# Kernel tuning notes

Hardware: AMD Instinct MI355X
Metric: run time of the kernel (lower is better)

## Reference

```python
import jax, jax.numpy as jnp
import numpy as np

D_MODEL = 2048
N_HEAD = 16
HEAD_DIM = D_MODEL // N_HEAD
SCALE = 1.0 / (HEAD_DIM ** 0.5)


def setup_inputs() -> dict:
    key = jax.random.key(0)
    kx, kq, kk, kv, ko = jax.random.split(key, 5)
    std = 1.0 / np.sqrt(D_MODEL)
    return {
        "x": jax.random.normal(kx, (2, 2048, D_MODEL), dtype=jnp.float32),
        "w_q": jax.random.normal(kq, (D_MODEL, D_MODEL), dtype=jnp.float32) * std,
        "w_k": jax.random.normal(kk, (D_MODEL, D_MODEL), dtype=jnp.float32) * std,
        "w_v": jax.random.normal(kv, (D_MODEL, D_MODEL), dtype=jnp.float32) * std,
        "w_o": jax.random.normal(ko, (D_MODEL, D_MODEL), dtype=jnp.float32) * std,
    }


def reference(x, w_q, w_k, w_v, w_o):
    b, s, d = x.shape
    # nn.Linear(d,d,bias=False): y = x @ W^T, weights stored [out, in]
    def proj(w):
        y = jnp.einsum("bsd,ed->bse", x, w)
        return y.reshape(b, s, N_HEAD, HEAD_DIM).transpose(0, 2, 1, 3)  # [b,h,s,hd]
    q, k, v = proj(w_q), proj(w_k), proj(w_v)
    scores = jnp.einsum("bhqd,bhkd->bhqk", q, k) * SCALE  # [b,h,s,s]
    probs = jax.nn.softmax(scores, axis=-1)
    attn = jnp.einsum("bhqk,bhkd->bhqd", probs, v)
    attn = attn.transpose(0, 2, 1, 3).reshape(b, s, d)
    return jnp.einsum("bsd,ed->bse", attn, w_o)
```

## Files before the change

### kernel.cpp

```cpp
#include <hip/hip_runtime.h>

#define D_MODEL 2048
#define SEQ 2048
#define BATCH 2
#define NH 16
#define HD 128
#define MTOT 4096
#define NQKV 6144
#define QSTRIDE 4096

static constexpr float SCALE_LOG2E = 0.08838834764831845f * 1.4426950408889634f;

typedef __bf16 bf16x8 __attribute__((ext_vector_type(8)));
typedef _Float16 f16x4 __attribute__((ext_vector_type(4)));
typedef float f32x4 __attribute__((ext_vector_type(4)));

__device__ inline unsigned short f2bf(float f) {
  unsigned int u = __builtin_bit_cast(unsigned int, f);
  u += 0x7fffu + ((u >> 16) & 1u);
  return (unsigned short)(u >> 16);
}

__device__ inline float fast_exp2(float x) {
#if __has_builtin(__builtin_amdgcn_exp2f)
  return __builtin_amdgcn_exp2f(x);
#else
  return exp2f(x);
#endif
}

__device__ inline void gload_lds16(const void* g, void* s) {
  __builtin_amdgcn_global_load_lds(
      (__attribute__((address_space(1))) void*)g,
      (__attribute__((address_space(3))) void*)s, 16, 0, 0);
}

__global__ __launch_bounds__(256) void cvt_all(
    const float* __restrict__ x, const float* __restrict__ wq,
    const float* __restrict__ wk, const float* __restrict__ wv,
    const float* __restrict__ wo, unsigned short* __restrict__ xb,
    unsigned short* __restrict__ wqkv, unsigned short* __restrict__ wob) {
  const int y = blockIdx.y;
  const float* src;
  unsigned short* dst;
  int n4;
  if (y == 0) { src = x; dst = xb; n4 = MTOT * D_MODEL / 4; }
  else if (y == 4) { src = wo; dst = wob; n4 = D_MODEL * D_MODEL / 4; }
  else {
    src = (y == 1) ? wq : (y == 2) ? wk : wv;
    dst = wqkv + (size_t)(y - 1) * D_MODEL * D_MODEL;
    n4 = D_MODEL * D_MODEL / 4;
  }
  int i = blockIdx.x * 256 + threadIdx.x;
  if (i < n4) {
    float4 v = ((const float4*)src)[i];
    ushort4 o;
    o.x = f2bf(v.x); o.y = f2bf(v.y); o.z = f2bf(v.z); o.w = f2bf(v.w);
    ((ushort4*)dst)[i] = o;
  }
}

__global__ __launch_bounds__(256, 2) void gemm_qkv(
    const unsigned short* __restrict__ A, const unsigned short* __restrict__ B,
    unsigned short* __restrict__ QK, unsigned short* __restrict__ Vt) {
  __shared__ __align__(16) union {
    struct { unsigned short As[128 * 32]; unsigned short Bs[128 * 32]; } s;
    unsigned short T[128 * 136];
  } u;
  unsigned short* As = u.s.As;
  unsigned short* Bs = u.s.Bs;
  const int K = D_MODEL;
  const int tid = threadIdx.x;
  const int lane = tid & 63;
  const int wave = tid >> 6;
  const int quad = lane >> 4;
  const int l15 = lane & 15;
  const int m0 = blockIdx.y * 128;
  const int n0 = blockIdx.x * 128;
  const int wm = (wave >> 1) * 64;
  const int wn = (wave & 1) * 64;

  const int c0 = wave * 2, c1 = wave * 2 + 1;
  const int srow = lane >> 2;
  const int sr0 = c0 * 16 + srow;
  const int sr1 = c1 * 16 + srow;
  const int sk = (((lane & 3) ^ (srow & 3))) * 8;
  const unsigned short* Ag0 = A + (size_t)(m0 + sr0) * K + sk;
  const unsigned short* Ag1 = A + (size_t)(m0 + sr1) * K + sk;
  const unsigned short* Bg0 = B + (size_t)(n0 + sr0) * K + sk;
  const unsigned short* Bg1 = B + (size_t)(n0 + sr1) * K + sk;
  unsigned short* lA0 = As + c0 * 512;
  unsigned short* lA1 = As + c1 * 512;
  unsigned short* lB0 = Bs + c0 * 512;
  unsigned short* lB1 = Bs + c1 * 512;

  f32x4 acc[4][4] = {};
  const int axor = (quad ^ (l15 & 3)) * 8;

  for (int k0 = 0; k0 < K; k0 += 32) {
    __syncthreads();
    gload_lds16(Ag0 + k0, lA0);
    gload_lds16(Ag1 + k0, lA1);
    gload_lds16(Bg0 + k0, lB0);
    gload_lds16(Bg1 + k0, lB1);
    __builtin_amdgcn_s_waitcnt(0);
    __syncthreads();
    bf16x8 a[4], b[4];
#pragma unroll
    for (int i = 0; i < 4; i++)
      a[i] = *(const bf16x8*)(As + (wm + i * 16 + l15) * 32 + axor);
#pragma unroll
    for (int j = 0; j < 4; j++)
      b[j] = *(const bf16x8*)(Bs + (wn + j * 16 + l15) * 32 + axor);
#pragma unroll
    for (int i = 0; i < 4; i++)
#pragma unroll
      for (int j = 0; j < 4; j++)
        acc[i][j] = __builtin_amdgcn_mfma_f32_16x16x32_bf16(a[i], b[j], acc[i][j], 0, 0, 0);
  }

  const int er = quad * 4;
  const int ec = l15;
  if (n0 < 4096) {
#pragma unroll
    for (int i = 0; i < 4; i++)
#pragma unroll
      for (int j = 0; j < 4; j++) {
        const int mm = m0 + wm + i * 16 + er;
        const int nn = n0 + wn + j * 16 + ec;
#pragma unroll
        for (int r = 0; r < 4; r++)
          QK[(size_t)(mm + r) * QSTRIDE + nn] = f2bf(acc[i][j][r]);
      }
  } else {
    __syncthreads();
    const int vcol0 = n0 - 4096;
    const int h = vcol0 >> 7;
    const int b = m0 >> 11;
    const int bh = b * NH + h;
    const int sbase = m0 & (SEQ - 1);
#pragma unroll
    for (int i = 0; i < 4; i++)
#pragma unroll
      for (int j = 0; j < 4; j++) {
        const int dl = wn + j * 16 + ec;
        const int sl = wm + i * 16 + er;
        f16x4 hv;
#pragma unroll
        for (int r = 0; r < 4; r++) hv[r] = (_Float16)acc[i][j][r];
        *(f16x4*)(u.T + dl * 136 + sl) = hv;
      }
    __syncthreads();
#pragma unroll
    for (int p = 0; p < 8; p++) {
      const int d = p * 16 + (tid >> 4);
      const int s = (tid & 15) * 8;
      float4 chunk = *(const float4*)(u.T + d * 136 + s);
      *(float4*)(Vt + ((size_t)(bh * HD + d)) * SEQ + sbase + s) = chunk;
    }
  }
}

__global__ __launch_bounds__(256, 4) void gemm_out(
    const unsigned short* __restrict__ A, const unsigned short* __restrict__ B,
    float* __restrict__ C, int M, int N, int K) {
  __shared__ __align__(16) unsigned short As[128 * 32];
  __shared__ __align__(16) unsigned short Bs[64 * 32];
  const int tid = threadIdx.x;
  const int lane = tid & 63;
  const int wave = tid >> 6;
  const int quad = lane >> 4;
  const int l15 = lane & 15;
  const int m0 = blockIdx.y * 128;
  const int n0 = blockIdx.x * 64;
  const int wm = (wave >> 1) * 64;
  const int wn = (wave & 1) * 32;

  const int srow = lane >> 2;
  const int sk = (((lane & 3) ^ (srow & 3))) * 8;
  const unsigned short* Ag0 = A + (size_t)(m0 + wave * 32 + srow) * K + sk;
  const unsigned short* Ag1 = A + (size_t)(m0 + wave * 32 + 16 + srow) * K + sk;
  unsigned short* lA0 = As + (wave * 2) * 512;
  unsigned short* lA1 = As + (wave * 2 + 1) * 512;
  const unsigned short* Bg = B + (size_t)(n0 + wave * 16 + srow) * K + sk;
  unsigned short* lB = Bs + wave * 512;

  f32x4 acc[4][2] = {};
  const int axor = (quad ^ (l15 & 3)) * 8;

  for (int k0 = 0; k0 < K; k0 += 32) {
    __syncthreads();
    gload_lds16(Ag0 + k0, lA0);
    gload_lds16(Ag1 + k0, lA1);
    gload_lds16(Bg + k0, lB);
    __builtin_amdgcn_s_waitcnt(0);
    __syncthreads();
    bf16x8 a[4], b[2];
#pragma unroll
    for (int i = 0; i < 4; i++)
      a[i] = *(const bf16x8*)(As + (wm + i * 16 + l15) * 32 + axor);
#pragma unroll
    for (int j = 0; j < 2; j++)
      b[j] = *(const bf16x8*)(Bs + (wn + j * 16 + l15) * 32 + axor);
#pragma unroll
    for (int i = 0; i < 4; i++)
#pragma unroll
      for (int j = 0; j < 2; j++)
        acc[i][j] = __builtin_amdgcn_mfma_f32_16x16x32_bf16(a[i], b[j], acc[i][j], 0, 0, 0);
  }

  const int er = quad * 4;
  const int ec = l15;
#pragma unroll
  for (int i = 0; i < 4; i++)
#pragma unroll
    for (int j = 0; j < 2; j++) {
      const int mm = m0 + wm + i * 16 + er;
      const int nn = n0 + wn + j * 16 + ec;
#pragma unroll
      for (int r = 0; r < 4; r++)
        C[(size_t)(mm + r) * N + nn] = acc[i][j][r];
    }
}

__global__ __launch_bounds__(256, 2) void flash_attn(
    const unsigned short* __restrict__ QK, const unsigned short* __restrict__ Vt,
    unsigned short* __restrict__ Og) {
  __shared__ __align__(16) unsigned short Ks[2][64 * 128];
  __shared__ __align__(16) unsigned short Vs[2][128 * 64];
  const int tid = threadIdx.x;
  const int lane = tid & 63;
  const int wave = tid >> 6;
  const int quad = lane >> 4;
  const int l15 = lane & 15;
  const int id = blockIdx.x;
  const int xr = id & 7;
  const int kk = id >> 3;
  const int bh = xr * 4 + (kk >> 4);
  const int b = bh >> 4, h = bh & 15;
  const int q0 = (kk & 15) * 128;

  const size_t kbase = (size_t)(b * SEQ) * QSTRIDE + D_MODEL + h * HD;
  const size_t vbase = (size_t)bh * HD * SEQ;

  bf16x8 qf[2][4];
#pragma unroll
  for (int t = 0; t < 2; t++)
#pragma unroll
    for (int kc = 0; kc < 4; kc++)
      qf[t][kc] = *(const bf16x8*)(QK + (size_t)(b * SEQ + q0 + wave * 32 + t * 16 + l15) * QSTRIDE +
                                   h * HD + kc * 32 + quad * 8);

  const unsigned short* kg[4];
  const unsigned short* vg[4];
  int klofs[4], vlofs[4];
#pragma unroll
  for (int i = 0; i < 4; i++) {
    int krow = wave * 16 + i * 4 + quad;
    int kc_ = l15 ^ (i * 4 + quad);
    kg[i] = QK + kbase + (size_t)krow * QSTRIDE + kc_ * 8;
    klofs[i] = (wave * 16 + i * 4) * 128;
    int vrow = wave * 32 + i * 8 + (lane >> 3);
    int vc_ = (lane & 7) ^ (lane >> 3);
    vg[i] = Vt + vbase + (size_t)vrow * SEQ + vc_ * 8;
    vlofs[i] = (wave * 32 + i * 8) * 64;
  }

#pragma unroll
  for (int i = 0; i < 4; i++) gload_lds16(kg[i], &Ks[0][klofs[i]]);
#pragma unroll
  for (int i = 0; i < 4; i++) gload_lds16(vg[i], &Vs[0][vlofs[i]]);
#pragma unroll
  for (int i = 0; i < 4; i++) { kg[i] += 64 * QSTRIDE; vg[i] += 64; }
  __builtin_amdgcn_s_waitcnt(0);
  __syncthreads();

  float lsum[2] = {0.f, 0.f};
  f32x4 Oa[2][8] = {};

  for (int it = 0; it < SEQ / 64; ++it) {
    const int cur = it & 1;
    if (it < SEQ / 64 - 1) {
#pragma unroll
      for (int i = 0; i < 4; i++) gload_lds16(kg[i], &Ks[cur ^ 1][klofs[i]]);
#pragma unroll
      for (int i = 0; i < 4; i++) gload_lds16(vg[i], &Vs[cur ^ 1][vlofs[i]]);
#pragma unroll
      for (int i = 0; i < 4; i++) { kg[i] += 64 * QSTRIDE; vg[i] += 64; }
    }

    const unsigned short* kb = &Ks[cur][0];
    f32x4 sacc[2][4] = {};
#pragma unroll
    for (int js = 0; js < 4; js++)
#pragma unroll
      for (int kc = 0; kc < 4; kc++) {
        bf16x8 kf = *(const bf16x8*)(kb + (js * 16 + l15) * 128 + (((kc * 4 + quad) ^ l15) * 8));
        sacc[0][js] = __builtin_amdgcn_mfma_f32_16x16x32_bf16(kf, qf[0][kc], sacc[0][js], 0, 0, 0);
        sacc[1][js] = __builtin_amdgcn_mfma_f32_16x16x32_bf16(kf, qf[1][kc], sacc[1][js], 0, 0, 0);
      }

    f16x4 pb[2][4];
#pragma unroll
    for (int t = 0; t < 2; t++)
#pragma unroll
      for (int js = 0; js < 4; js++)
#pragma unroll
        for (int r = 0; r < 4; r++) {
          float p = fast_exp2(sacc[t][js][r] * SCALE_LOG2E);
          lsum[t] += p;
          pb[t][js][r] = (_Float16)p;
        }

    const unsigned short* vb_ = &Vs[cur][0];
#pragma unroll
    for (int jt = 0; jt < 8; jt++)
#pragma unroll
      for (int js = 0; js < 4; js++) {
        f16x4 vf = *(const f16x4*)(vb_ + (jt * 16 + l15) * 64 +
                                   (((js * 2 + (quad >> 1)) ^ (lane & 7)) * 8) + (quad & 1) * 4);
        Oa[0][jt] = __builtin_amdgcn_mfma_f32_16x16x16f16(vf, pb[0][js], Oa[0][jt], 0, 0, 0);
        Oa[1][jt] = __builtin_amdgcn_mfma_f32_16x16x16f16(vf, pb[1][js], Oa[1][jt], 0, 0, 0);
      }

    __builtin_amdgcn_s_waitcnt(0);
    __syncthreads();
  }

  float inv[2];
#pragma unroll
  for (int t = 0; t < 2; t++) {
    float s = lsum[t];
    s += __shfl_xor(s, 16);
    s += __shfl_xor(s, 32);
    inv[t] = 1.0f / s;
  }

#pragma unroll
  for (int t = 0; t < 2; t++) {
    const size_t rowbase = (size_t)(b * SEQ + q0 + wave * 32 + t * 16 + l15) * D_MODEL + h * HD;
#pragma unroll
    for (int jt = 0; jt < 8; jt++) {
      ushort4 o;
      o.x = f2bf(Oa[t][jt][0] * inv[t]);
      o.y = f2bf(Oa[t][jt][1] * inv[t]);
      o.z = f2bf(Oa[t][jt][2] * inv[t]);
      o.w = f2bf(Oa[t][jt][3] * inv[t]);
      *(ushort4*)(Og + rowbase + jt * 16 + quad * 4) = o;
    }
  }
}

extern "C" void kernel_launch(void* const* d_in, const int* in_sizes, int n_in,
                              void* d_out, int out_size, void* d_ws, size_t ws_size,
                              hipStream_t stream) {
  const float* x = (const float*)d_in[0];
  const float* wq = (const float*)d_in[1];
  const float* wk = (const float*)d_in[2];
  const float* wv = (const float*)d_in[3];
  const float* wo = (const float*)d_in[4];
  float* out = (float*)d_out;
  char* ws = (char*)d_ws;
  const size_t MB = 1u << 20;
  if (ws_size < 96 * MB) return;

  unsigned short* xb = (unsigned short*)(ws);
  unsigned short* wqkv = (unsigned short*)(ws + 16 * MB);
  unsigned short* wob = (unsigned short*)(ws + 40 * MB);
  unsigned short* QKb = (unsigned short*)(ws + 48 * MB);
  unsigned short* Vtb = (unsigned short*)(ws + 80 * MB);
  unsigned short* Ab = xb;

  cvt_all<<<dim3(8192, 5), 256, 0, stream>>>(x, wq, wk, wv, wo, xb, wqkv, wob);

  gemm_qkv<<<dim3(NQKV / 128, MTOT / 128), 256, 0, stream>>>(xb, wqkv, QKb, Vtb);

  flash_attn<<<512, 256, 0, stream>>>(QKb, Vtb, Ab);

  gemm_out<<<dim3(D_MODEL / 64, MTOT / 128), 256, 0, stream>>>(Ab, wob, out, MTOT, D_MODEL, D_MODEL);
}
```

Before: 397.3 us.

## Rewrite QKV GEMM as 256x256 tiles with double-buffered LDS ping-pong pipeline

Replaces the 128x128, single-buffered, fully synchronous QKV GEMM with a 512-thread kernel that computes 256x256 tiles, uses 64-wide K steps and 128 KB of dynamic LDS in two buffers. Global-to-LDS loads for the next stage are interleaved with MFMA phases under barriers and setprio, so memory latency is meant to overlap with matrix math and per-tile data reuse rises. The V transpose epilogue is reworked to handle two heads per tile in two passes. In exchange, occupancy drops to one large block per CU, with 384 blocks that may not fill the GPU evenly, and the hand-built wait and barrier choreography is fragile.

```diff
diff --git a/kernel.cpp b/kernel.cpp
--- a/kernel.cpp
+++ b/kernel.cpp
@@ -60,105 +60,160 @@
   }
 }
 
-__global__ __launch_bounds__(256, 2) void gemm_qkv(
+__global__ __launch_bounds__(512, 2) void gemm_qkv(
     const unsigned short* __restrict__ A, const unsigned short* __restrict__ B,
     unsigned short* __restrict__ QK, unsigned short* __restrict__ Vt) {
-  __shared__ __align__(16) union {
-    struct { unsigned short As[128 * 32]; unsigned short Bs[128 * 32]; } s;
-    unsigned short T[128 * 136];
-  } u;
-  unsigned short* As = u.s.As;
-  unsigned short* Bs = u.s.Bs;
+  extern __shared__ __align__(16) char smem[];
   const int K = D_MODEL;
   const int tid = threadIdx.x;
   const int lane = tid & 63;
   const int wave = tid >> 6;
   const int quad = lane >> 4;
   const int l15 = lane & 15;
-  const int m0 = blockIdx.y * 128;
-  const int n0 = blockIdx.x * 128;
-  const int wm = (wave >> 1) * 64;
-  const int wn = (wave & 1) * 64;
-
-  const int c0 = wave * 2, c1 = wave * 2 + 1;
-  const int srow = lane >> 2;
-  const int sr0 = c0 * 16 + srow;
-  const int sr1 = c1 * 16 + srow;
-  const int sk = (((lane & 3) ^ (srow & 3))) * 8;
-  const unsigned short* Ag0 = A + (size_t)(m0 + sr0) * K + sk;
-  const unsigned short* Ag1 = A + (size_t)(m0 + sr1) * K + sk;
-  const unsigned short* Bg0 = B + (size_t)(n0 + sr0) * K + sk;
-  const unsigned short* Bg1 = B + (size_t)(n0 + sr1) * K + sk;
-  unsigned short* lA0 = As + c0 * 512;
-  unsigned short* lA1 = As + c1 * 512;
-  unsigned short* lB0 = Bs + c0 * 512;
-  unsigned short* lB1 = Bs + c1 * 512;
-
-  f32x4 acc[4][4] = {};
-  const int axor = (quad ^ (l15 & 3)) * 8;
-
-  for (int k0 = 0; k0 < K; k0 += 32) {
-    __syncthreads();
-    gload_lds16(Ag0 + k0, lA0);
-    gload_lds16(Ag1 + k0, lA1);
-    gload_lds16(Bg0 + k0, lB0);
-    gload_lds16(Bg1 + k0, lB1);
-    __builtin_amdgcn_s_waitcnt(0);
-    __syncthreads();
-    bf16x8 a[4], b[4];
-#pragma unroll
-    for (int i = 0; i < 4; i++)
-      a[i] = *(const bf16x8*)(As + (wm + i * 16 + l15) * 32 + axor);
-#pragma unroll
-    for (int j = 0; j < 4; j++)
-      b[j] = *(const bf16x8*)(Bs + (wn + j * 16 + l15) * 32 + axor);
-#pragma unroll
-    for (int i = 0; i < 4; i++)
-#pragma unroll
-      for (int j = 0; j < 4; j++)
-        acc[i][j] = __builtin_amdgcn_mfma_f32_16x16x32_bf16(a[i], b[j], acc[i][j], 0, 0, 0);
+  const int bid = blockIdx.x;
+  const int tm = bid / (NQKV / 256);
+  const int tn = bid % (NQKV / 256);
+  const int m0 = tm * 256;
+  const int n0 = tn * 256;
+  const int wm = wave >> 2;
+  const int wn = wave & 3;
+
+  const int srow = wave * 16 + (lane >> 3);
+  const int cch = ((lane & 7) ^ (lane >> 3)) * 8;
+  const unsigned short* As0 = A + (size_t)(m0 + srow) * K + cch;
+  const unsigned short* As1 = As0 + (size_t)8 * K;
+  const unsigned short* Bs0 = B + (size_t)(n0 + srow) * K + cch;
+  const unsigned short* Bs1 = Bs0 + (size_t)8 * K;
+  const size_t HS = (size_t)128 * K;
+  char* ldst = smem + wave * 2048;
+
+#define STAGE(s0, s1, kofs, ldsofs)                       \
+  do {                                                    \
+    gload_lds16((s0) + (kofs), ldst + (ldsofs));          \
+    gload_lds16((s1) + (kofs), ldst + (ldsofs) + 1024);   \
+  } while (0)
+
+  const int arow = (wm * 128 + l15) * 128;
+  const int brow = (wn * 64 + l15) * 128;
+  const int sk0 = (quad ^ (l15 & 7)) * 16;
+  const int sk1 = ((4 + quad) ^ (l15 & 7)) * 16;
+
+  f32x4 acc[8][4] = {};
+  bf16x8 a[4][2], bl[2][2], bh[2][2];
+
+#define LDA(p, mb)                                                             \
+  _Pragma("unroll") for (int mi = 0; mi < 4; mi++) {                           \
+    a[mi][0] = *(const bf16x8*)(smem + (p) * 65536 + arow + ((mb) + mi) * 2048 + sk0); \
+    a[mi][1] = *(const bf16x8*)(smem + (p) * 65536 + arow + ((mb) + mi) * 2048 + sk1); \
+  }
+#define LDB(p, B_, nb)                                                         \
+  _Pragma("unroll") for (int ni = 0; ni < 2; ni++) {                           \
+    B_[ni][0] = *(const bf16x8*)(smem + (p) * 65536 + 32768 + brow + ((nb) + ni) * 2048 + sk0); \
+    B_[ni][1] = *(const bf16x8*)(smem + (p) * 65536 + 32768 + brow + ((nb) + ni) * 2048 + sk1); \
+  }
+#define MMA(mh, B_, nh)                                                        \
+  _Pragma("unroll") for (int mi = 0; mi < 4; mi++)                             \
+  _Pragma("unroll") for (int ni = 0; ni < 2; ni++) {                           \
+    acc[(mh) * 4 + mi][(nh) * 2 + ni] = __builtin_amdgcn_mfma_f32_16x16x32_bf16( \
+        a[mi][0], B_[ni][0], acc[(mh) * 4 + mi][(nh) * 2 + ni], 0, 0, 0);      \
+    acc[(mh) * 4 + mi][(nh) * 2 + ni] = __builtin_amdgcn_mfma_f32_16x16x32_bf16( \
+        a[mi][1], B_[ni][1], acc[(mh) * 4 + mi][(nh) * 2 + ni], 0, 0, 0);      \
+  }
+#define BARX() __builtin_amdgcn_s_barrier()
+#define PRIO(x) __builtin_amdgcn_s_setprio(x)
+#define VMCNT4() asm volatile("s_waitcnt vmcnt(4)" ::: "memory")
+
+  STAGE(As0, As1, 0, 0);
+  STAGE(As0 + HS, As1 + HS, 0, 16384);
+  STAGE(Bs0, Bs1, 0, 32768);
+  STAGE(Bs0 + HS, Bs1 + HS, 0, 49152);
+  STAGE(Bs0, Bs1, 64, 65536 + 32768);
+  STAGE(Bs0 + HS, Bs1 + HS, 64, 65536 + 49152);
+  VMCNT4();
+  BARX();
+
+  for (int i = 0; i < K / 128; ++i) {
+    const int kO = ((2 * i + 1) & 31) * 64;
+    const int kE = ((2 * i + 2) & 31) * 64;
+    const int kO3 = ((2 * i + 3) & 31) * 64;
+    LDA(0, 0); LDB(0, bl, 0);
+    STAGE(As0, As1, kO, 65536);
+    BARX(); PRIO(1); MMA(0, bl, 0); PRIO(0); BARX();
+    LDB(0, bh, 2);
+    STAGE(As0 + HS, As1 + HS, kO, 65536 + 16384);
+    BARX(); PRIO(1); MMA(0, bh, 1); PRIO(0); BARX();
+    LDA(0, 4);
+    STAGE(Bs0, Bs1, kE, 32768);
+    BARX(); PRIO(1); MMA(1, bl, 0); PRIO(0); BARX();
+    STAGE(Bs0 + HS, Bs1 + HS, kE, 49152);
+    BARX(); PRIO(1); MMA(1, bh, 1); PRIO(0); VMCNT4(); BARX();
+    LDA(1, 0); LDB(1, bl, 0);
+    STAGE(As0, As1, kE, 0);
+    BARX(); PRIO(1); MMA(0, bl, 0); PRIO(0); BARX();
+    LDB(1, bh, 2);
+    STAGE(As0 + HS, As1 + HS, kE, 16384);
+    BARX(); PRIO(1); MMA(0, bh, 1); PRIO(0); BARX();
+    LDA(1, 4);
+    STAGE(Bs0, Bs1, kO3, 65536 + 32768);
+    BARX(); PRIO(1); MMA(1, bl, 0); PRIO(0); BARX();
+    STAGE(Bs0 + HS, Bs1 + HS, kO3, 65536 + 49152);
+    BARX(); PRIO(1); MMA(1, bh, 1); PRIO(0); VMCNT4(); BARX();
   }
 
   const int er = quad * 4;
-  const int ec = l15;
   if (n0 < 4096) {
 #pragma unroll
-    for (int i = 0; i < 4; i++)
-#pragma unroll
-      for (int j = 0; j < 4; j++) {
-        const int mm = m0 + wm + i * 16 + er;
-        const int nn = n0 + wn + j * 16 + ec;
+    for (int mi = 0; mi < 8; mi++)
+#pragma unroll
+      for (int ni = 0; ni < 4; ni++) {
+        const int mm = m0 + wm * 128 + mi * 16 + er;
+        const int nn = n0 + wn * 64 + ni * 16 + l15;
 #pragma unroll
         for (int r = 0; r < 4; r++)
-          QK[(size_t)(mm + r) * QSTRIDE + nn] = f2bf(acc[i][j][r]);
+          QK[(size_t)(mm + r) * QSTRIDE + nn] = f2bf(acc[mi][ni][r]);
       }
   } else {
-    __syncthreads();
+    asm volatile("s_waitcnt vmcnt(0)" ::: "memory");
+    BARX();
+    unsigned short* T = (unsigned short*)smem;
     const int vcol0 = n0 - 4096;
-    const int h = vcol0 >> 7;
-    const int b = m0 >> 11;
-    const int bh = b * NH + h;
+    const int bb = m0 >> 11;
+    const int h0 = vcol0 >> 7;
     const int sbase = m0 & (SEQ - 1);
 #pragma unroll
-    for (int i = 0; i < 4; i++)
-#pragma unroll
-      for (int j = 0; j < 4; j++) {
-        const int dl = wn + j * 16 + ec;
-        const int sl = wm + i * 16 + er;
-        f16x4 hv;
-#pragma unroll
-        for (int r = 0; r < 4; r++) hv[r] = (_Float16)acc[i][j][r];
-        *(f16x4*)(u.T + dl * 136 + sl) = hv;
+    for (int p = 0; p < 2; p++) {
+      if (p) BARX();
+      if ((wn >> 1) == p) {
+#pragma unroll
+        for (int mi = 0; mi < 8; mi++)
+#pragma unroll
+          for (int ni = 0; ni < 4; ni++) {
+            const int d = (wn & 1) * 64 + ni * 16 + l15;
+            const int s = wm * 128 + mi * 16 + er;
+            f16x4 hv;
+#pragma unroll
+            for (int r = 0; r < 4; r++) hv[r] = (_Float16)acc[mi][ni][r];
+            *(f16x4*)(T + d * 264 + s) = hv;
+          }
       }
-    __syncthreads();
-#pragma unroll
-    for (int p = 0; p < 8; p++) {
-      const int d = p * 16 + (tid >> 4);
-      const int s = (tid & 15) * 8;
-      float4 chunk = *(const float4*)(u.T + d * 136 + s);
-      *(float4*)(Vt + ((size_t)(bh * HD + d)) * SEQ + sbase + s) = chunk;
+      BARX();
+      const int d = tid >> 2;
+      const int sc = (tid & 3) * 64;
+      const size_t vrow = ((size_t)(bb * NH + h0 + p) * HD + d) * SEQ + sbase + sc;
+#pragma unroll
+      for (int j = 0; j < 8; j++) {
+        float4 c4 = *(const float4*)(T + d * 264 + sc + j * 8);
+        *(float4*)(Vt + vrow + j * 8) = c4;
+      }
     }
   }
+#undef STAGE
+#undef LDA
+#undef LDB
+#undef MMA
+#undef BARX
+#undef PRIO
+#undef VMCNT4
 }
 
 __global__ __launch_bounds__(256, 4) void gemm_out(
@@ -371,9 +426,16 @@
   unsigned short* Vtb = (unsigned short*)(ws + 80 * MB);
   unsigned short* Ab = xb;
 
+  static int lds_set = 0;
+  if (!lds_set) {
+    hipFuncSetAttribute((const void*)gemm_qkv,
+                        hipFuncAttributeMaxDynamicSharedMemorySize, 131072);
+    lds_set = 1;
+  }
+
   cvt_all<<<dim3(8192, 5), 256, 0, stream>>>(x, wq, wk, wv, wo, xb, wqkv, wob);
 
-  gemm_qkv<<<dim3(NQKV / 128, MTOT / 128), 256, 0, stream>>>(xb, wqkv, QKb, Vtb);
+  gemm_qkv<<<dim3((NQKV / 256) * (MTOT / 256)), 512, 131072, stream>>>(xb, wqkv, QKb, Vtb);
 
   flash_attn<<<512, 256, 0, stream>>>(QKb, Vtb, Ab);
 
```

Measured after the change: 388.4 us. -2.2%, faster.

## Rewrite projection GEMMs with 256x128 tiles, triple-buffered LDS pipeline

Applied to the files above, without the earlier changes.

Both projection GEMMs now use 512-thread blocks computing 256x128 tiles with K-step 64. A triple-buffered dynamic LDS pipeline (144KB) prefetches two tiles ahead using direct global-to-LDS loads, split barriers, setprio around MFMA bursts and XOR-swizzled LDS reads. Blocks are remapped in an XCD-aware order, replacing the old single-buffered 128x32 loop that stalled on every load. The cost is heavy LDS use (likely one block per CU despite launch bounds of 2) and fewer blocks for gemm_out.

```diff
diff --git a/kernel.cpp b/kernel.cpp
--- a/kernel.cpp
+++ b/kernel.cpp
@@ -60,166 +60,165 @@
   }
 }
 
-__global__ __launch_bounds__(256, 2) void gemm_qkv(
+#define GEMM_SETUP(Aptr, Bptr)                                                 \
+  const int tid = threadIdx.x;                                                 \
+  const int lane = tid & 63;                                                   \
+  const int wave = tid >> 6;                                                   \
+  const int quad = lane >> 4;                                                  \
+  const int l15 = lane & 15;                                                   \
+  const int wm = wave >> 1;                                                    \
+  const int wn = wave & 1;                                                     \
+  const unsigned short* Ag =                                                   \
+      (Aptr) + (size_t)(m0 + wave * 8 + (lane >> 3)) * 2048 +                  \
+      (size_t)(((lane & 7) ^ (lane >> 3)) * 8);                                \
+  const unsigned short* Bg =                                                   \
+      (Bptr) + (size_t)(n0 + wave * 8 + (lane >> 3)) * 2048 +                  \
+      (size_t)(((lane & 7) ^ (lane >> 3)) * 8);                                \
+  char* sd = smem + wave * 1024;                                               \
+  const int arow0 = (wm * 64 + l15) * 128;                                     \
+  const int brow0 = (wn * 64 + l15) * 128;                                     \
+  const int sk0 = ((quad) ^ (l15 & 7)) * 16;                                   \
+  const int sk1 = ((4 + quad) ^ (l15 & 7)) * 16;                               \
+  f32x4 acc[4][4] = {};
+
+#define SA(tt, u, NB)                                                          \
+  gload_lds16(Ag + (size_t)(u) * 64 * 2048 + (tt) * 64,                        \
+              sd + (NB) * 49152 + (u) * 8192)
+#define SB(tt, u, NB)                                                          \
+  gload_lds16(Bg + (size_t)(u) * 64 * 2048 + (tt) * 64,                        \
+              sd + (NB) * 49152 + 32768 + (u) * 8192)
+
+#define RDA(dst, mi, CB)                                                       \
+  dst[0] = *(const bf16x8*)(smem + (CB) * 49152 + arow0 + (mi) * 2048 + sk0);  \
+  dst[1] = *(const bf16x8*)(smem + (CB) * 49152 + arow0 + (mi) * 2048 + sk1);
+#define RDB(ni, CB)                                                            \
+  bfr[ni][0] =                                                                 \
+      *(const bf16x8*)(smem + (CB) * 49152 + 32768 + brow0 + (ni) * 2048 + sk0); \
+  bfr[ni][1] =                                                                 \
+      *(const bf16x8*)(smem + (CB) * 49152 + 32768 + brow0 + (ni) * 2048 + sk1);
+
+#define MM2(mi, areg)                                                          \
+  _Pragma("unroll") for (int ni_ = 0; ni_ < 4; ni_++) {                        \
+    acc[mi][ni_] = __builtin_amdgcn_mfma_f32_16x16x32_bf16(                    \
+        areg[0], bfr[ni_][0], acc[mi][ni_], 0, 0, 0);                          \
+    acc[mi][ni_] = __builtin_amdgcn_mfma_f32_16x16x32_bf16(                    \
+        areg[1], bfr[ni_][1], acc[mi][ni_], 0, 0, 0);                          \
+  }
+
+#define TILE(t, CB, NB, DOSTAGE, VMN)                                          \
+  {                                                                            \
+    bf16x8 af0[2], af1[2], af2[2], af3[2], bfr[4][2];                          \
+    RDA(af0, 0, CB); RDA(af1, 1, CB);                                          \
+    RDB(0, CB); RDB(1, CB); RDB(2, CB); RDB(3, CB);                            \
+    if (DOSTAGE) { SA((t) + 2, 0, NB); SA((t) + 2, 1, NB); SB((t) + 2, 0, NB); } \
+    __builtin_amdgcn_s_barrier();                                              \
+    asm volatile("s_waitcnt lgkmcnt(0)" ::: "memory");                         \
+    __builtin_amdgcn_sched_barrier(0);                                         \
+    __builtin_amdgcn_s_setprio(1);                                             \
+    MM2(0, af0); MM2(1, af1);                                                  \
+    __builtin_amdgcn_s_setprio(0);                                             \
+    __builtin_amdgcn_s_barrier();                                              \
+    RDA(af2, 2, CB); RDA(af3, 3, CB);                                          \
+    if (DOSTAGE) { SA((t) + 2, 2, NB); SA((t) + 2, 3, NB); SB((t) + 2, 1, NB); } \
+    __builtin_amdgcn_s_barrier();                                              \
+    asm volatile("s_waitcnt lgkmcnt(0)" ::: "memory");                         \
+    __builtin_amdgcn_sched_barrier(0);                                         \
+    __builtin_amdgcn_s_setprio(1);                                             \
+    MM2(2, af2); MM2(3, af3);                                                  \
+    __builtin_amdgcn_s_setprio(0);                                             \
+    asm volatile("s_waitcnt vmcnt(" #VMN ")" ::: "memory");                    \
+    __builtin_amdgcn_s_barrier();                                              \
+  }
+
+#define GEMM_KLOOP()                                                           \
+  SA(0, 0, 0); SA(0, 1, 0); SA(0, 2, 0); SA(0, 3, 0); SB(0, 0, 0); SB(0, 1, 0);\
+  SA(1, 0, 1); SA(1, 1, 1); SA(1, 2, 1); SA(1, 3, 1); SB(1, 0, 1); SB(1, 1, 1);\
+  asm volatile("s_waitcnt vmcnt(6)" ::: "memory");                             \
+  __builtin_amdgcn_s_barrier();                                                \
+  for (int t = 0; t < 30; t += 3) {                                            \
+    TILE(t + 0, 0, 2, 1, 6);                                                   \
+    TILE(t + 1, 1, 0, 1, 6);                                                   \
+    TILE(t + 2, 2, 1, 1, 6);                                                   \
+  }                                                                            \
+  TILE(30, 0, 2, 0, 0);                                                        \
+  TILE(31, 1, 0, 0, 0);
+
+__global__ __launch_bounds__(512, 2) void gemm_qkv(
     const unsigned short* __restrict__ A, const unsigned short* __restrict__ B,
     unsigned short* __restrict__ QK, unsigned short* __restrict__ Vt) {
-  __shared__ __align__(16) union {
-    struct { unsigned short As[128 * 32]; unsigned short Bs[128 * 32]; } s;
-    unsigned short T[128 * 136];
-  } u;
-  unsigned short* As = u.s.As;
-  unsigned short* Bs = u.s.Bs;
-  const int K = D_MODEL;
-  const int tid = threadIdx.x;
-  const int lane = tid & 63;
-  const int wave = tid >> 6;
-  const int quad = lane >> 4;
-  const int l15 = lane & 15;
-  const int m0 = blockIdx.y * 128;
-  const int n0 = blockIdx.x * 128;
-  const int wm = (wave >> 1) * 64;
-  const int wn = (wave & 1) * 64;
-
-  const int c0 = wave * 2, c1 = wave * 2 + 1;
-  const int srow = lane >> 2;
-  const int sr0 = c0 * 16 + srow;
-  const int sr1 = c1 * 16 + srow;
-  const int sk = (((lane & 3) ^ (srow & 3))) * 8;
-  const unsigned short* Ag0 = A + (size_t)(m0 + sr0) * K + sk;
-  const unsigned short* Ag1 = A + (size_t)(m0 + sr1) * K + sk;
-  const unsigned short* Bg0 = B + (size_t)(n0 + sr0) * K + sk;
-  const unsigned short* Bg1 = B + (size_t)(n0 + sr1) * K + sk;
-  unsigned short* lA0 = As + c0 * 512;
-  unsigned short* lA1 = As + c1 * 512;
-  unsigned short* lB0 = Bs + c0 * 512;
-  unsigned short* lB1 = Bs + c1 * 512;
-
-  f32x4 acc[4][4] = {};
-  const int axor = (quad ^ (l15 & 3)) * 8;
-
-  for (int k0 = 0; k0 < K; k0 += 32) {
-    __syncthreads();
-    gload_lds16(Ag0 + k0, lA0);
-    gload_lds16(Ag1 + k0, lA1);
-    gload_lds16(Bg0 + k0, lB0);
-    gload_lds16(Bg1 + k0, lB1);
-    __builtin_amdgcn_s_waitcnt(0);
-    __syncthreads();
-    bf16x8 a[4], b[4];
-#pragma unroll
-    for (int i = 0; i < 4; i++)
-      a[i] = *(const bf16x8*)(As + (wm + i * 16 + l15) * 32 + axor);
-#pragma unroll
-    for (int j = 0; j < 4; j++)
-      b[j] = *(const bf16x8*)(Bs + (wn + j * 16 + l15) * 32 + axor);
-#pragma unroll
-    for (int i = 0; i < 4; i++)
-#pragma unroll
-      for (int j = 0; j < 4; j++)
-        acc[i][j] = __builtin_amdgcn_mfma_f32_16x16x32_bf16(a[i], b[j], acc[i][j], 0, 0, 0);
-  }
-
-  const int er = quad * 4;
-  const int ec = l15;
+  extern __shared__ __align__(16) char smem[];
+  const int bid = blockIdx.x;
+  const int wgid = (bid & 7) * 96 + (bid >> 3);
+  const int tm = wgid / 48;
+  const int tn = wgid - tm * 48;
+  const int m0 = tm * 256;
+  const int n0 = tn * 128;
+  GEMM_SETUP(A, B);
+  GEMM_KLOOP();
+
   if (n0 < 4096) {
 #pragma unroll
-    for (int i = 0; i < 4; i++)
-#pragma unroll
-      for (int j = 0; j < 4; j++) {
-        const int mm = m0 + wm + i * 16 + er;
-        const int nn = n0 + wn + j * 16 + ec;
+    for (int mi = 0; mi < 4; mi++)
+#pragma unroll
+      for (int ni = 0; ni < 4; ni++) {
+        const int mm = m0 + wm * 64 + mi * 16 + quad * 4;
+        const int nn = n0 + wn * 64 + ni * 16 + l15;
 #pragma unroll
         for (int r = 0; r < 4; r++)
-          QK[(size_t)(mm + r) * QSTRIDE + nn] = f2bf(acc[i][j][r]);
+          QK[(size_t)(mm + r) * QSTRIDE + nn] = f2bf(acc[mi][ni][r]);
       }
   } else {
-    __syncthreads();
-    const int vcol0 = n0 - 4096;
-    const int h = vcol0 >> 7;
-    const int b = m0 >> 11;
-    const int bh = b * NH + h;
+    asm volatile("s_waitcnt vmcnt(0)" ::: "memory");
+    __builtin_amdgcn_s_barrier();
+    unsigned short* T = (unsigned short*)smem;
+    const int h = (n0 - 4096) >> 7;
+    const int bb = m0 >> 11;
     const int sbase = m0 & (SEQ - 1);
 #pragma unroll
-    for (int i = 0; i < 4; i++)
-#pragma unroll
-      for (int j = 0; j < 4; j++) {
-        const int dl = wn + j * 16 + ec;
-        const int sl = wm + i * 16 + er;
+    for (int mi = 0; mi < 4; mi++)
+#pragma unroll
+      for (int ni = 0; ni < 4; ni++) {
+        const int d = wn * 64 + ni * 16 + l15;
+        const int s = wm * 64 + mi * 16 + quad * 4;
         f16x4 hv;
 #pragma unroll
-        for (int r = 0; r < 4; r++) hv[r] = (_Float16)acc[i][j][r];
-        *(f16x4*)(u.T + dl * 136 + sl) = hv;
+        for (int r = 0; r < 4; r++) hv[r] = (_Float16)acc[mi][ni][r];
+        *(f16x4*)(T + d * 264 + s) = hv;
       }
-    __syncthreads();
-#pragma unroll
-    for (int p = 0; p < 8; p++) {
-      const int d = p * 16 + (tid >> 4);
-      const int s = (tid & 15) * 8;
-      float4 chunk = *(const float4*)(u.T + d * 136 + s);
-      *(float4*)(Vt + ((size_t)(bh * HD + d)) * SEQ + sbase + s) = chunk;
+    __builtin_amdgcn_s_barrier();
+    const int d = tid >> 2;
+    const int sc = (tid & 3) * 64;
+    const size_t vrow = ((size_t)(bb * NH + h) * HD + d) * SEQ + sbase + sc;
+#pragma unroll
+    for (int j = 0; j < 8; j++) {
+      float4 c4 = *(const float4*)(T + d * 264 + sc + j * 8);
+      *(float4*)(Vt + vrow + j * 8) = c4;
     }
   }
 }
 
-__global__ __launch_bounds__(256, 4) void gemm_out(
+__global__ __launch_bounds__(512, 2) void gemm_out(
     const unsigned short* __restrict__ A, const unsigned short* __restrict__ B,
-    float* __restrict__ C, int M, int N, int K) {
-  __shared__ __align__(16) unsigned short As[128 * 32];
-  __shared__ __align__(16) unsigned short Bs[64 * 32];
-  const int tid = threadIdx.x;
-  const int lane = tid & 63;
-  const int wave = tid >> 6;
-  const int quad = lane >> 4;
-  const int l15 = lane & 15;
-  const int m0 = blockIdx.y * 128;
-  const int n0 = blockIdx.x * 64;
-  const int wm = (wave >> 1) * 64;
-  const int wn = (wave & 1) * 32;
-
-  const int srow = lane >> 2;
-  const int sk = (((lane & 3) ^ (srow & 3))) * 8;
-  const unsigned short* Ag0 = A + (size_t)(m0 + wave * 32 + srow) * K + sk;
-  const unsigned short* Ag1 = A + (size_t)(m0 + wave * 32 + 16 + srow) * K + sk;
-  unsigned short* lA0 = As + (wave * 2) * 512;
-  unsigned short* lA1 = As + (wave * 2 + 1) * 512;
-  const unsigned short* Bg = B + (size_t)(n0 + wave * 16 + srow) * K + sk;
-  unsigned short* lB = Bs + wave * 512;
-
-  f32x4 acc[4][2] = {};
-  const int axor = (quad ^ (l15 & 3)) * 8;
-
-  for (int k0 = 0; k0 < K; k0 += 32) {
-    __syncthreads();
-    gload_lds16(Ag0 + k0, lA0);
-    gload_lds16(Ag1 + k0, lA1);
-    gload_lds16(Bg + k0, lB);
-    __builtin_amdgcn_s_waitcnt(0);
-    __syncthreads();
-    bf16x8 a[4], b[2];
-#pragma unroll
-    for (int i = 0; i < 4; i++)
-      a[i] = *(const bf16x8*)(As + (wm + i * 16 + l15) * 32 + axor);
-#pragma unroll
-    for (int j = 0; j < 2; j++)
-      b[j] = *(const bf16x8*)(Bs + (wn + j * 16 + l15) * 32 + axor);
-#pragma unroll
-    for (int i = 0; i < 4; i++)
-#pragma unroll
-      for (int j = 0; j < 2; j++)
-        acc[i][j] = __builtin_amdgcn_mfma_f32_16x16x32_bf16(a[i], b[j], acc[i][j], 0, 0, 0);
-  }
-
-  const int er = quad * 4;
-  const int ec = l15;
-#pragma unroll
-  for (int i = 0; i < 4; i++)
-#pragma unroll
-    for (int j = 0; j < 2; j++) {
-      const int mm = m0 + wm + i * 16 + er;
-      const int nn = n0 + wn + j * 16 + ec;
+    float* __restrict__ C) {
+  extern __shared__ __align__(16) char smem[];
+  const int bid = blockIdx.x;
+  const int wgid = (bid & 7) * 32 + (bid >> 3);
+  const int tm = wgid >> 4;
+  const int tn = wgid & 15;
+  const int m0 = tm * 256;
+  const int n0 = tn * 128;
+  GEMM_SETUP(A, B);
+  GEMM_KLOOP();
+
+#pragma unroll
+  for (int mi = 0; mi < 4; mi++)
+#pragma unroll
+    for (int ni = 0; ni < 4; ni++) {
+      const int mm = m0 + wm * 64 + mi * 16 + quad * 4;
+      const int nn = n0 + wn * 64 + ni * 16 + l15;
 #pragma unroll
       for (int r = 0; r < 4; r++)
-        C[(size_t)(mm + r) * N + nn] = acc[i][j][r];
+        C[(size_t)(mm + r) * D_MODEL + nn] = acc[mi][ni][r];
     }
 }
 
@@ -371,11 +370,20 @@
   unsigned short* Vtb = (unsigned short*)(ws + 80 * MB);
   unsigned short* Ab = xb;
 
+  static int lds_set = 0;
+  if (!lds_set) {
+    hipFuncSetAttribute((const void*)gemm_qkv,
+                        hipFuncAttributeMaxDynamicSharedMemorySize, 147456);
+    hipFuncSetAttribute((const void*)gemm_out,
+                        hipFuncAttributeMaxDynamicSharedMemorySize, 147456);
+    lds_set = 1;
+  }
+
   cvt_all<<<dim3(8192, 5), 256, 0, stream>>>(x, wq, wk, wv, wo, xb, wqkv, wob);
 
-  gemm_qkv<<<dim3(NQKV / 128, MTOT / 128), 256, 0, stream>>>(xb, wqkv, QKb, Vtb);
+  gemm_qkv<<<768, 512, 147456, stream>>>(xb, wqkv, QKb, Vtb);
 
   flash_attn<<<512, 256, 0, stream>>>(QKb, Vtb, Ab);
 
-  gemm_out<<<dim3(D_MODEL / 64, MTOT / 128), 256, 0, stream>>>(Ab, wob, out, MTOT, D_MODEL, D_MODEL);
-}
+  gemm_out<<<256, 512, 147456, stream>>>(Ab, wob, out);
+}
```

New measurement: 359.9 us. 1.1x faster.
